# Kernel optimization log

Hardware: AMD Instinct MI355X
Metric: run time of the kernel (lower is better)

## Reference

```python
import jax, jax.numpy as jnp
import numpy as np

B, T, D = 4, 2048, 1024
H = 16
DK = D // H


def setup_inputs() -> dict:
    key = jax.random.key(0)
    k1, k2, k3, k4 = jax.random.split(key, 4)
    x = jax.random.normal(k1, (B, T, D), dtype=jnp.float32)
    prefix_lengths = jax.random.randint(k2, (B,), 0, 1024, dtype=jnp.int64)
    # torch Linear weights: [out_features, in_features], scaled like kaiming-uniform-ish
    W_qkv = jax.random.normal(k3, (3 * D, D), dtype=jnp.float32) / np.sqrt(D)
    W_o = jax.random.normal(k4, (D, D), dtype=jnp.float32) / np.sqrt(D)
    return {"x": x, "prefix_lengths": prefix_lengths, "W_qkv": W_qkv, "W_o": W_o}


def _prefix_lm_mask(seq_len, prefix_lengths):
    # True where attention is BLOCKED.
    pos = jnp.arange(seq_len)
    key_pos = pos[None, None, :]          # [1,1,T]
    query_pos = pos[None, :, None]        # [1,T,1]
    prefix = prefix_lengths[:, None, None]  # [B,1,1]
    q_in_pre = query_pos < prefix
    k_in_pre = key_pos < prefix
    block_pre_to_suf = q_in_pre & ~k_in_pre
    block_future_suf = ~q_in_pre & ~k_in_pre & (key_pos > query_pos)
    return block_pre_to_suf | block_future_suf  # [B,T,T]


def reference(x, prefix_lengths, W_qkv, W_o):
    Bb, Tt, Cc = x.shape
    qkv = x @ W_qkv.T                     # [B,T,3D]
    qkv = qkv.reshape(Bb, Tt, 3, H, DK).transpose(2, 0, 3, 1, 4)  # [3,B,H,T,dk]
    q, k, v = qkv[0], qkv[1], qkv[2]
    scale = 1.0 / np.sqrt(DK).astype(np.float32)
    attn = jnp.einsum('bhqd,bhkd->bhqk', q, k) * scale  # [B,H,T,T]
    pl = jnp.clip(prefix_lengths.astype(jnp.int32), 0, Tt)
    mask = _prefix_lm_mask(Tt, pl)        # [B,T,T]
    attn = jnp.where(mask[:, None, :, :], -jnp.inf, attn)
    attn = jax.nn.softmax(attn, axis=-1)
    out = jnp.einsum('bhqk,bhkd->bhqd', attn, v)  # [B,H,T,dk]
    out = out.transpose(0, 2, 1, 3).reshape(Bb, Tt, Cc)
    return out @ W_o.T
```

## Files before the change

kernel.cpp:

```cpp
#include <hip/hip_runtime.h>
#include <stdint.h>

#define NB 4
#define NT 2048
#define ND 1024
#define NH 16
#define NDK 64
#define NTD 3072

typedef __attribute__((ext_vector_type(8))) short short8;
typedef __attribute__((ext_vector_type(4))) float f32x4;
typedef unsigned short u16;
typedef unsigned int u32;

__device__ __forceinline__ u16 f2bf(float f) {
    u32 u = __builtin_bit_cast(u32, f);
    u += 0x7fffu + ((u >> 16) & 1u);
    return (u16)(u >> 16);
}
__device__ __forceinline__ float bf2f(u16 s) {
    u32 u = ((u32)s) << 16;
    return __builtin_bit_cast(float, u);
}

__device__ __forceinline__ void gl_lds16(const u16* g, u16* l) {
    __builtin_amdgcn_global_load_lds(
        (const __attribute__((address_space(1))) u32*)g,
        (__attribute__((address_space(3))) u32*)l, 16, 0, 0);
}

__device__ __forceinline__ int swz(int row, int col) {
    return row * 32 + ((((col >> 3) ^ (row >> 1) ^ (row >> 3)) & 3) << 3) + (col & 7);
}

__global__ __launch_bounds__(256) void cvt_all(const float* __restrict__ x,
                                               const float* __restrict__ wqkv,
                                               const float* __restrict__ wo,
                                               u16* __restrict__ xb,
                                               u16* __restrict__ wqb,
                                               u16* __restrict__ wob) {
    const int n0 = NB * NT * ND;
    const int n1 = 3 * ND * ND;
    int i = (blockIdx.x * 256 + threadIdx.x) * 8;
    const float* src;
    u16* dst;
    if (i < n0) {
        src = x + i; dst = xb + i;
    } else if (i < n0 + n1) {
        src = wqkv + (i - n0); dst = wqb + (i - n0);
    } else {
        src = wo + (i - n0 - n1); dst = wob + (i - n0 - n1);
    }
    float4 a = *(const float4*)(src);
    float4 b = *(const float4*)(src + 4);
    short8 r;
    r[0] = (short)f2bf(a.x); r[1] = (short)f2bf(a.y);
    r[2] = (short)f2bf(a.z); r[3] = (short)f2bf(a.w);
    r[4] = (short)f2bf(b.x); r[5] = (short)f2bf(b.y);
    r[6] = (short)f2bf(b.z); r[7] = (short)f2bf(b.w);
    *(short8*)(dst) = r;
}

template <typename OutT>
__global__ __launch_bounds__(256) void gemm_bt(const u16* __restrict__ A,
                                               const u16* __restrict__ Bm,
                                               OutT* __restrict__ C,
                                               int M, int N, int K) {
    __shared__ __align__(16) u16 As[128 * 32];
    __shared__ __align__(16) u16 Bs[128 * 32];
    const int tid  = threadIdx.x;
    const int wave = tid >> 6, lane = tid & 63;
    const int quad = lane >> 4, l16 = lane & 15;
    const int wm = wave >> 1, wn = wave & 1;
    const int row0 = blockIdx.x * 128, col0 = blockIdx.y * 128;

    f32x4 acc[4][4];
#pragma unroll
    for (int i = 0; i < 4; ++i)
#pragma unroll
        for (int j = 0; j < 4; ++j) acc[i][j] = (f32x4){0.f, 0.f, 0.f, 0.f};

    const u16* Ag = A + (size_t)(row0 + (tid >> 2)) * K + ((tid & 3) * 8);
    const u16* Bg = Bm + (size_t)(col0 + (tid >> 2)) * K + ((tid & 3) * 8);
    const size_t stride64 = (size_t)64 * K;
    u16* As0 = As + wave * 512;
    u16* As1 = As + 2048 + wave * 512;
    u16* Bs0 = Bs + wave * 512;
    u16* Bs1 = Bs + 2048 + wave * 512;

    for (int k0 = 0; k0 < K; k0 += 32) {
        gl_lds16(Ag + k0, As0);
        gl_lds16(Ag + k0 + stride64, As1);
        gl_lds16(Bg + k0, Bs0);
        gl_lds16(Bg + k0 + stride64, Bs1);
        __syncthreads();
        short8 af[4], bfr[4];
#pragma unroll
        for (int mi = 0; mi < 4; ++mi)
            af[mi] = *(const short8*)&As[(wm * 64 + mi * 16 + l16) * 32 + quad * 8];
#pragma unroll
        for (int ni = 0; ni < 4; ++ni)
            bfr[ni] = *(const short8*)&Bs[(wn * 64 + ni * 16 + l16) * 32 + quad * 8];
#pragma unroll
        for (int mi = 0; mi < 4; ++mi)
#pragma unroll
            for (int ni = 0; ni < 4; ++ni)
                acc[mi][ni] = __builtin_amdgcn_mfma_f32_16x16x32_bf16(
                    af[mi], bfr[ni], acc[mi][ni], 0, 0, 0);
        __syncthreads();
    }

#pragma unroll
    for (int mi = 0; mi < 4; ++mi) {
#pragma unroll
        for (int ni = 0; ni < 4; ++ni) {
            const int r = row0 + wm * 64 + mi * 16 + quad * 4;
            const int c = col0 + wn * 64 + ni * 16 + l16;
#pragma unroll
            for (int rr = 0; rr < 4; ++rr) {
                float v = acc[mi][ni][rr];
                if constexpr (sizeof(OutT) == 2)
                    C[(size_t)(r + rr) * N + c] = (OutT)f2bf(v);
                else
                    C[(size_t)(r + rr) * N + c] = (OutT)v;
            }
        }
    }
}

__global__ __launch_bounds__(256) void transpose_v(const u16* __restrict__ qkv,
                                                   u16* __restrict__ vt) {
    __shared__ __align__(16) u16 L[64 * 72];
    const int tid = threadIdx.x;
    const int bh = blockIdx.x, b = bh >> 4, h = bh & 15;
    const int t0 = blockIdx.y * 64;
    const u16* Vg = qkv + ((size_t)(b * NT + t0)) * NTD + 2 * ND + h * NDK;

    const int trow = tid >> 3, g = tid & 7;
#pragma unroll
    for (int rep = 0; rep < 2; ++rep) {
        const int t = trow + rep * 32;
        short8 v = *(const short8*)(Vg + (size_t)t * NTD + g * 8);
        *(short8*)&L[t * 72 + ((g ^ (t & 7)) << 3)] = v;
    }
    __syncthreads();
    const int d = tid & 63, w = tid >> 6;
    u16* O = vt + ((size_t)bh * 64 + d) * NT + t0;
#pragma unroll
    for (int rep = 0; rep < 2; ++rep) {
        const int c = w + rep * 4;
        short8 o;
#pragma unroll
        for (int j = 0; j < 8; ++j) {
            const int t = c * 8 + j;
            o[j] = L[t * 72 + ((((d >> 3) ^ (t & 7)) << 3)) + (d & 7)];
        }
        *(short8*)(O + c * 8) = o;
    }
}

__global__ __launch_bounds__(256) void flash_prefix(const u16* __restrict__ qkv,
                                                    const u16* __restrict__ vt,
                                                    const int* __restrict__ plen,
                                                    u16* __restrict__ attn) {
    __shared__ __align__(16) u16 Vt2[2][2048];
    __shared__ __align__(16) u16 Kt2[2][2048];
    __shared__ __align__(16) u16 Pl[4 * 512];

    const int tid  = threadIdx.x;
    const int wave = tid >> 6, lane = tid & 63;
    const int quad = lane >> 4, l16 = lane & 15;
    const int bh = blockIdx.x, b = bh >> 4, h = bh & 15;
    const int q0 = blockIdx.y * 64;

    int P;
    {
        bool is64 = (plen[1] == 0) && (plen[3] == 0);
        P = is64 ? plen[2 * b] : plen[b];
        P = P < 0 ? 0 : (P > NT ? NT : P);
    }

    const u16* Qg = qkv + (size_t)b * NT * NTD + h * NDK;
    const u16* Kg = Qg + ND;
    const u16* Vtb = vt + (size_t)bh * 64 * NT;

    const int qbase = q0 + wave * 16;
    u16* Pw = Pl + wave * 512;

    const float QSCALE = 0.18033688f;

    const int va = tid;
    const int vrow = va >> 2;
    const int vtq = (va ^ (vrow >> 1) ^ (vrow >> 3)) & 3;
    const u16* vsrc = Vtb + (size_t)vrow * NT + vtq * 8;
    const int ka = tid;
    const int krow = ka >> 3;
    const int kc = (ka ^ krow) & 7;
    const u16* ksrc = Kg + (size_t)krow * NTD + kc * 8;
    const int ldsoff = wave * 512;

    short8 qa[2];
#pragma unroll
    for (int kd = 0; kd < 2; ++kd) {
        short8 tq = *(const short8*)(Qg + (size_t)(qbase + l16) * NTD + kd * 32 + quad * 8);
#pragma unroll
        for (int j = 0; j < 8; ++j)
            tq[j] = (short)f2bf(bf2f((u16)tq[j]) * QSCALE);
        qa[kd] = tq;
    }

    short8 ones;
#pragma unroll
    for (int j = 0; j < 8; ++j) ones[j] = (short)0x3F80;

    f32x4 o[4];
#pragma unroll
    for (int nt = 0; nt < 4; ++nt) o[nt] = (f32x4){0.f, 0.f, 0.f, 0.f};
    f32x4 lsum = (f32x4){0.f, 0.f, 0.f, 0.f};

    int kl[4];
#pragma unroll
    for (int rr = 0; rr < 4; ++rr) {
        const int qrow = qbase + quad * 4 + rr;
        kl[rr] = (qrow < P) ? P : (qrow + 1);
    }
    const int klmin = (qbase < P) ? P : (qbase + 1);
    const int kmax = (q0 + 64 > P) ? (q0 + 64) : P;

    gl_lds16(vsrc, &Vt2[0][ldsoff]);
    gl_lds16(ksrc, &Kt2[0][ldsoff]);
    int buf = 0;

    for (int k0 = 0; k0 < kmax; k0 += 32) {
        __syncthreads();
        if (k0 + 32 < kmax) {
            gl_lds16(vsrc + (k0 + 32), &Vt2[buf ^ 1][ldsoff]);
            gl_lds16(ksrc + (size_t)(k0 + 32) * NTD, &Kt2[buf ^ 1][ldsoff]);
        }
        const u16* Kb = Kt2[buf];
        const u16* Vb = Vt2[buf];

        f32x4 s[2];
#pragma unroll
        for (int ni = 0; ni < 2; ++ni) {
            s[ni] = (f32x4){0.f, 0.f, 0.f, 0.f};
#pragma unroll
            for (int kd = 0; kd < 2; ++kd) {
                const int r = ni * 16 + l16;
                const short8 kb = *(const short8*)&Kb[r * 64 + ((((kd * 4 + quad) ^ r) & 7) << 3)];
                s[ni] = __builtin_amdgcn_mfma_f32_16x16x32_bf16(qa[kd], kb, s[ni], 0, 0, 0);
            }
        }

        const bool full = (k0 + 32 <= klmin);
#pragma unroll
        for (int ni = 0; ni < 2; ++ni) {
#pragma unroll
            for (int rr = 0; rr < 4; ++rr) {
                float sv = s[ni][rr];
                if (!full) {
                    const int kpos = k0 + ni * 16 + l16;
                    sv = (kpos < kl[rr]) ? sv : -1e30f;
                }
                const float p = exp2f(sv);
                const u32 u = __builtin_bit_cast(u32, p) + 0x8000u;
                Pw[swz(quad * 4 + rr, ni * 16 + l16)] = (u16)(u >> 16);
            }
        }

        const short8 pa = *(const short8*)&Pw[swz(l16, quad * 8)];
        lsum = __builtin_amdgcn_mfma_f32_16x16x32_bf16(pa, ones, lsum, 0, 0, 0);
#pragma unroll
        for (int nt = 0; nt < 4; ++nt) {
            const short8 vb = *(const short8*)&Vb[swz(nt * 16 + l16, quad * 8)];
            o[nt] = __builtin_amdgcn_mfma_f32_16x16x32_bf16(pa, vb, o[nt], 0, 0, 0);
        }
        buf ^= 1;
    }

#pragma unroll
    for (int rr = 0; rr < 4; ++rr) {
        const float inv = 1.0f / lsum[rr];
        const size_t rowoff = (size_t)(b * NT + qbase + quad * 4 + rr) * ND + h * NDK;
#pragma unroll
        for (int nt = 0; nt < 4; ++nt)
            attn[rowoff + nt * 16 + l16] = f2bf(o[nt][rr] * inv);
    }
}

extern "C" void kernel_launch(void* const* d_in, const int* in_sizes, int n_in,
                              void* d_out, int out_size, void* d_ws, size_t ws_size,
                              hipStream_t stream) {
    const float* x    = (const float*)d_in[0];
    const int*   plen = (const int*)d_in[1];
    const float* wqkv = (const float*)d_in[2];
    const float* wo   = (const float*)d_in[3];
    float* out = (float*)d_out;

    char* ws = (char*)d_ws;
    u16* xb   = (u16*)(ws);
    u16* wqb  = (u16*)(ws + 16777216);
    u16* wob  = (u16*)(ws + 23068672);
    u16* qkv  = (u16*)(ws + 25165824);
    u16* attn = (u16*)(ws + 75497472);
    u16* vtb  = (u16*)(ws + 92274688);

    cvt_all<<<6144, 256, 0, stream>>>(x, wqkv, wo, xb, wqb, wob);

    gemm_bt<u16><<<dim3(64, 24), 256, 0, stream>>>(xb, wqb, qkv, NB * NT, 3 * ND, ND);

    transpose_v<<<dim3(64, 32), 256, 0, stream>>>(qkv, vtb);

    flash_prefix<<<dim3(64, 32), 256, 0, stream>>>(qkv, vtb, plen, attn);

    gemm_bt<float><<<dim3(64, 8), 256, 0, stream>>>(attn, wob, out, NB * NT, ND, ND);
}
```

Before: 300.1 us.

## Split key range across wave pairs with 32-query tiles and LDS reduction

Each block now covers 32 query rows instead of 64. The four waves form two pairs that each process half of a 64-key tile, and their partial outputs and row sums are combined through LDS at the end. The grid doubles and is launched in reverse query order so the long causal blocks start first, which should improve load balance and occupancy. The cost is an extra LDS reduction and barrier, and K/V tiles are loaded twice as often per query row.

```diff
diff --git a/kernel.cpp b/kernel.cpp
--- a/kernel.cpp
+++ b/kernel.cpp
@@ -163,15 +163,16 @@
                                                     const u16* __restrict__ vt,
                                                     const int* __restrict__ plen,
                                                     u16* __restrict__ attn) {
-    __shared__ __align__(16) u16 Vt2[2][2048];
-    __shared__ __align__(16) u16 Kt2[2][2048];
+    __shared__ __align__(16) u16 Kt2[2][4096];
+    __shared__ __align__(16) u16 Vt2[2][4096];
     __shared__ __align__(16) u16 Pl[4 * 512];
 
     const int tid  = threadIdx.x;
     const int wave = tid >> 6, lane = tid & 63;
     const int quad = lane >> 4, l16 = lane & 15;
+    const int pair = wave >> 1, rg = wave & 1;
     const int bh = blockIdx.x, b = bh >> 4, h = bh & 15;
-    const int q0 = blockIdx.y * 64;
+    const int q0 = (63 - blockIdx.y) * 32;
 
     int P;
     {
@@ -184,20 +185,15 @@
     const u16* Kg = Qg + ND;
     const u16* Vtb = vt + (size_t)bh * 64 * NT;
 
-    const int qbase = q0 + wave * 16;
+    const int qbase = q0 + rg * 16;
     u16* Pw = Pl + wave * 512;
-
     const float QSCALE = 0.18033688f;
 
-    const int va = tid;
-    const int vrow = va >> 2;
-    const int vtq = (va ^ (vrow >> 1) ^ (vrow >> 3)) & 3;
-    const u16* vsrc = Vtb + (size_t)vrow * NT + vtq * 8;
-    const int ka = tid;
-    const int krow = ka >> 3;
-    const int kc = (ka ^ krow) & 7;
-    const u16* ksrc = Kg + (size_t)krow * NTD + kc * 8;
-    const int ldsoff = wave * 512;
+    const int krow = tid >> 3, kch = (tid ^ krow) & 7;
+    const u16* ksp = Kg + (size_t)krow * NTD + kch * 8;
+    const int vd = tid >> 3, vch = (tid ^ vd) & 7;
+    const u16* vsp = Vtb + (size_t)vd * NT + vch * 8;
+    const int koff = wave * 512;
 
     short8 qa[2];
 #pragma unroll
@@ -225,17 +221,25 @@
         kl[rr] = (qrow < P) ? P : (qrow + 1);
     }
     const int klmin = (qbase < P) ? P : (qbase + 1);
-    const int kmax = (q0 + 64 > P) ? (q0 + 64) : P;
-
-    gl_lds16(vsrc, &Vt2[0][ldsoff]);
-    gl_lds16(ksrc, &Kt2[0][ldsoff]);
+    const int kmax = (q0 + 32 > P) ? (q0 + 32) : P;
+
+    gl_lds16(ksp, &Kt2[0][koff]);
+    gl_lds16(ksp + (size_t)32 * NTD, &Kt2[0][2048 + koff]);
+    gl_lds16(vsp, &Vt2[0][koff]);
+    gl_lds16(vsp + (size_t)32 * NT, &Vt2[0][2048 + koff]);
+    const u16* ksn = ksp + (size_t)64 * NTD;
+    const u16* vsn = vsp + 64;
     int buf = 0;
 
-    for (int k0 = 0; k0 < kmax; k0 += 32) {
+    for (int k0 = 0; k0 < kmax; k0 += 64) {
         __syncthreads();
-        if (k0 + 32 < kmax) {
-            gl_lds16(vsrc + (k0 + 32), &Vt2[buf ^ 1][ldsoff]);
-            gl_lds16(ksrc + (size_t)(k0 + 32) * NTD, &Kt2[buf ^ 1][ldsoff]);
+        if (k0 + 64 < kmax) {
+            gl_lds16(ksn, &Kt2[buf ^ 1][koff]);
+            gl_lds16(ksn + (size_t)32 * NTD, &Kt2[buf ^ 1][2048 + koff]);
+            gl_lds16(vsn, &Vt2[buf ^ 1][koff]);
+            gl_lds16(vsn + (size_t)32 * NT, &Vt2[buf ^ 1][2048 + koff]);
+            ksn += (size_t)64 * NTD;
+            vsn += 64;
         }
         const u16* Kb = Kt2[buf];
         const u16* Vb = Vt2[buf];
@@ -244,22 +248,22 @@
 #pragma unroll
         for (int ni = 0; ni < 2; ++ni) {
             s[ni] = (f32x4){0.f, 0.f, 0.f, 0.f};
+            const int r = pair * 32 + ni * 16 + l16;
 #pragma unroll
             for (int kd = 0; kd < 2; ++kd) {
-                const int r = ni * 16 + l16;
-                const short8 kb = *(const short8*)&Kb[r * 64 + ((((kd * 4 + quad) ^ r) & 7) << 3)];
+                const short8 kb = *(const short8*)&Kb[r * 64 + ((((kd * 4 + quad) ^ (l16 & 7)) & 7) << 3)];
                 s[ni] = __builtin_amdgcn_mfma_f32_16x16x32_bf16(qa[kd], kb, s[ni], 0, 0, 0);
             }
         }
 
-        const bool full = (k0 + 32 <= klmin);
+        const bool full = (k0 + pair * 32 + 32 <= klmin);
 #pragma unroll
         for (int ni = 0; ni < 2; ++ni) {
 #pragma unroll
             for (int rr = 0; rr < 4; ++rr) {
                 float sv = s[ni][rr];
                 if (!full) {
-                    const int kpos = k0 + ni * 16 + l16;
+                    const int kpos = k0 + pair * 32 + ni * 16 + l16;
                     sv = (kpos < kl[rr]) ? sv : -1e30f;
                 }
                 const float p = exp2f(sv);
@@ -272,19 +276,47 @@
         lsum = __builtin_amdgcn_mfma_f32_16x16x32_bf16(pa, ones, lsum, 0, 0, 0);
 #pragma unroll
         for (int nt = 0; nt < 4; ++nt) {
-            const short8 vb = *(const short8*)&Vb[swz(nt * 16 + l16, quad * 8)];
+            const int d = nt * 16 + l16;
+            const short8 vb = *(const short8*)&Vb[d * 64 + ((((pair * 4 + quad) ^ (l16 & 7)) & 7) << 3)];
             o[nt] = __builtin_amdgcn_mfma_f32_16x16x32_bf16(pa, vb, o[nt], 0, 0, 0);
         }
         buf ^= 1;
     }
 
-#pragma unroll
-    for (int rr = 0; rr < 4; ++rr) {
-        const float inv = 1.0f / lsum[rr];
-        const size_t rowoff = (size_t)(b * NT + qbase + quad * 4 + rr) * ND + h * NDK;
+    __syncthreads();
+    float* comb = (float*)&Kt2[0][0];
+    if (wave >= 2) {
+        float* cw = comb + (wave - 2) * 1056;
 #pragma unroll
         for (int nt = 0; nt < 4; ++nt)
-            attn[rowoff + nt * 16 + l16] = f2bf(o[nt][rr] * inv);
+#pragma unroll
+            for (int rr = 0; rr < 4; ++rr)
+                cw[(quad * 4 + rr) * 65 + nt * 16 + l16] = o[nt][rr];
+        if (l16 == 0) {
+#pragma unroll
+            for (int rr = 0; rr < 4; ++rr)
+                cw[1040 + quad * 4 + rr] = lsum[rr];
+        }
+    }
+    __syncthreads();
+    if (wave < 2) {
+        const float* cw = comb + wave * 1056;
+#pragma unroll
+        for (int rr = 0; rr < 4; ++rr)
+            lsum[rr] += cw[1040 + quad * 4 + rr];
+#pragma unroll
+        for (int nt = 0; nt < 4; ++nt)
+#pragma unroll
+            for (int rr = 0; rr < 4; ++rr)
+                o[nt][rr] += cw[(quad * 4 + rr) * 65 + nt * 16 + l16];
+#pragma unroll
+        for (int rr = 0; rr < 4; ++rr) {
+            const float inv = 1.0f / lsum[rr];
+            const size_t rowoff = (size_t)(b * NT + qbase + quad * 4 + rr) * ND + h * NDK;
+#pragma unroll
+            for (int nt = 0; nt < 4; ++nt)
+                attn[rowoff + nt * 16 + l16] = f2bf(o[nt][rr] * inv);
+        }
     }
 }
 
@@ -311,7 +343,7 @@
 
     transpose_v<<<dim3(64, 32), 256, 0, stream>>>(qkv, vtb);
 
-    flash_prefix<<<dim3(64, 32), 256, 0, stream>>>(qkv, vtb, plen, attn);
+    flash_prefix<<<dim3(64, 64), 256, 0, stream>>>(qkv, vtb, plen, attn);
 
     gemm_bt<float><<<dim3(64, 8), 256, 0, stream>>>(attn, wob, out, NB * NT, ND, ND);
 }
```

Result: slower. 308.3 us (+2.7%).

## Fuse V transpose into QKV GEMM epilogue and use persistent atomic scheduling for attention

Applied to the files above, without the earlier changes.

The separate transpose_v kernel is removed. A specialized QKV GEMM writes the V columns straight into a transposed layout through an LDS staging step in its epilogue. The flash attention kernel becomes persistent with 1024 blocks, and each block takes tasks from a global atomic counter, starting with the longest query tiles, to balance the triangular causal workload. This costs an extra memset, an atomic per task, and a counter placed just before the attn buffer in the workspace.

```diff
diff --git a/kernel.cpp b/kernel.cpp
--- a/kernel.cpp
+++ b/kernel.cpp
@@ -128,163 +128,233 @@
     }
 }
 
-__global__ __launch_bounds__(256) void transpose_v(const u16* __restrict__ qkv,
-                                                   u16* __restrict__ vt) {
-    __shared__ __align__(16) u16 L[64 * 72];
-    const int tid = threadIdx.x;
-    const int bh = blockIdx.x, b = bh >> 4, h = bh & 15;
-    const int t0 = blockIdx.y * 64;
-    const u16* Vg = qkv + ((size_t)(b * NT + t0)) * NTD + 2 * ND + h * NDK;
-
-    const int trow = tid >> 3, g = tid & 7;
-#pragma unroll
-    for (int rep = 0; rep < 2; ++rep) {
-        const int t = trow + rep * 32;
-        short8 v = *(const short8*)(Vg + (size_t)t * NTD + g * 8);
-        *(short8*)&L[t * 72 + ((g ^ (t & 7)) << 3)] = v;
-    }
-    __syncthreads();
-    const int d = tid & 63, w = tid >> 6;
-    u16* O = vt + ((size_t)bh * 64 + d) * NT + t0;
-#pragma unroll
-    for (int rep = 0; rep < 2; ++rep) {
-        const int c = w + rep * 4;
-        short8 o;
-#pragma unroll
-        for (int j = 0; j < 8; ++j) {
-            const int t = c * 8 + j;
-            o[j] = L[t * 72 + ((((d >> 3) ^ (t & 7)) << 3)) + (d & 7)];
-        }
-        *(short8*)(O + c * 8) = o;
+__global__ __launch_bounds__(256) void gemm_qkv(const u16* __restrict__ A,
+                                                const u16* __restrict__ Bm,
+                                                u16* __restrict__ Cq,
+                                                u16* __restrict__ vtb) {
+    const int Kd = ND, Nn = NTD;
+    __shared__ __align__(16) u16 As[128 * 32];
+    __shared__ __align__(16) u16 Bs[128 * 32];
+    const int tid  = threadIdx.x;
+    const int wave = tid >> 6, lane = tid & 63;
+    const int quad = lane >> 4, l16 = lane & 15;
+    const int wm = wave >> 1, wn = wave & 1;
+    const int row0 = blockIdx.x * 128, col0 = blockIdx.y * 128;
+
+    f32x4 acc[4][4];
+#pragma unroll
+    for (int i = 0; i < 4; ++i)
+#pragma unroll
+        for (int j = 0; j < 4; ++j) acc[i][j] = (f32x4){0.f, 0.f, 0.f, 0.f};
+
+    const u16* Ag = A + (size_t)(row0 + (tid >> 2)) * Kd + ((tid & 3) * 8);
+    const u16* Bg = Bm + (size_t)(col0 + (tid >> 2)) * Kd + ((tid & 3) * 8);
+    const size_t stride64 = (size_t)64 * Kd;
+    u16* As0 = As + wave * 512;
+    u16* As1 = As + 2048 + wave * 512;
+    u16* Bs0 = Bs + wave * 512;
+    u16* Bs1 = Bs + 2048 + wave * 512;
+
+    for (int k0 = 0; k0 < Kd; k0 += 32) {
+        gl_lds16(Ag + k0, As0);
+        gl_lds16(Ag + k0 + stride64, As1);
+        gl_lds16(Bg + k0, Bs0);
+        gl_lds16(Bg + k0 + stride64, Bs1);
+        __syncthreads();
+        short8 af[4], bfr[4];
+#pragma unroll
+        for (int mi = 0; mi < 4; ++mi)
+            af[mi] = *(const short8*)&As[(wm * 64 + mi * 16 + l16) * 32 + quad * 8];
+#pragma unroll
+        for (int ni = 0; ni < 4; ++ni)
+            bfr[ni] = *(const short8*)&Bs[(wn * 64 + ni * 16 + l16) * 32 + quad * 8];
+#pragma unroll
+        for (int mi = 0; mi < 4; ++mi)
+#pragma unroll
+            for (int ni = 0; ni < 4; ++ni)
+                acc[mi][ni] = __builtin_amdgcn_mfma_f32_16x16x32_bf16(
+                    af[mi], bfr[ni], acc[mi][ni], 0, 0, 0);
+        __syncthreads();
+    }
+
+    if (col0 < 2048) {
+#pragma unroll
+        for (int mi = 0; mi < 4; ++mi)
+#pragma unroll
+            for (int ni = 0; ni < 4; ++ni) {
+                const int r = row0 + wm * 64 + mi * 16 + quad * 4;
+                const int c = col0 + wn * 64 + ni * 16 + l16;
+#pragma unroll
+                for (int rr = 0; rr < 4; ++rr)
+                    Cq[(size_t)(r + rr) * Nn + c] = f2bf(acc[mi][ni][rr]);
+            }
+    } else {
+        const int hb = ((col0 - 2048) >> 6) + wn;
+        const int bq = (row0 + wm * 64) >> 11;
+        const int tb = (row0 + wm * 64) & 2047;
+        u16* Ovt = vtb + (size_t)(bq * NH + hb) * 64 * NT + tb;
+#pragma unroll
+        for (int phase = 0; phase < 2; ++phase) {
+            __syncthreads();
+            if ((wave >> 1) == phase) {
+                u16* L = (wave & 1) ? Bs : As;
+#pragma unroll
+                for (int mi = 0; mi < 4; ++mi) {
+                    const int r4 = mi * 4 + quad;
+#pragma unroll
+                    for (int ni = 0; ni < 4; ++ni) {
+                        const int cl = ni * 16 + l16;
+                        u32 lo = (u32)f2bf(acc[mi][ni][0]) | ((u32)f2bf(acc[mi][ni][1]) << 16);
+                        u32 hi = (u32)f2bf(acc[mi][ni][2]) | ((u32)f2bf(acc[mi][ni][3]) << 16);
+                        u32* p = (u32*)&L[cl * 64 + (((r4 ^ cl) & 15) << 2)];
+                        p[0] = lo; p[1] = hi;
+                    }
+                }
+#pragma unroll
+                for (int rep = 0; rep < 8; ++rep) {
+                    const int cl = (lane >> 3) + rep * 8;
+                    const int tc = lane & 7;
+                    const u32* p0 = (const u32*)&L[cl * 64 + ((((2 * tc) ^ cl) & 15) << 2)];
+                    const u32* p1 = (const u32*)&L[cl * 64 + ((((2 * tc + 1) ^ cl) & 15) << 2)];
+                    u32 o0 = p0[0], o1 = p0[1], o2 = p1[0], o3 = p1[1];
+                    u32* q = (u32*)(Ovt + (size_t)cl * NT + tc * 8);
+                    q[0] = o0; q[1] = o1; q[2] = o2; q[3] = o3;
+                }
+            }
+        }
     }
 }
 
 __global__ __launch_bounds__(256) void flash_prefix(const u16* __restrict__ qkv,
                                                     const u16* __restrict__ vt,
                                                     const int* __restrict__ plen,
-                                                    u16* __restrict__ attn) {
+                                                    u16* __restrict__ attn,
+                                                    u32* __restrict__ ctr) {
     __shared__ __align__(16) u16 Vt2[2][2048];
     __shared__ __align__(16) u16 Kt2[2][2048];
     __shared__ __align__(16) u16 Pl[4 * 512];
+    __shared__ int taskS;
 
     const int tid  = threadIdx.x;
     const int wave = tid >> 6, lane = tid & 63;
     const int quad = lane >> 4, l16 = lane & 15;
-    const int bh = blockIdx.x, b = bh >> 4, h = bh & 15;
-    const int q0 = blockIdx.y * 64;
-
-    int P;
-    {
-        bool is64 = (plen[1] == 0) && (plen[3] == 0);
-        P = is64 ? plen[2 * b] : plen[b];
+    const float QSCALE = 0.18033688f;
+    const int ldsoff = wave * 512;
+
+    short8 ones;
+#pragma unroll
+    for (int j = 0; j < 8; ++j) ones[j] = (short)0x3F80;
+
+    const bool is64 = (plen[1] == 0) && (plen[3] == 0);
+
+    for (;;) {
+        if (tid == 0) taskS = (int)atomicAdd(ctr, 1u);
+        __syncthreads();
+        const int task = taskS;
+        if (task >= 2048) break;
+
+        const int bh = task & 63, b = bh >> 4, h = bh & 15;
+        const int q0 = (31 - (task >> 6)) * 64;
+
+        int P = is64 ? plen[2 * b] : plen[b];
         P = P < 0 ? 0 : (P > NT ? NT : P);
-    }
-
-    const u16* Qg = qkv + (size_t)b * NT * NTD + h * NDK;
-    const u16* Kg = Qg + ND;
-    const u16* Vtb = vt + (size_t)bh * 64 * NT;
-
-    const int qbase = q0 + wave * 16;
-    u16* Pw = Pl + wave * 512;
-
-    const float QSCALE = 0.18033688f;
-
-    const int va = tid;
-    const int vrow = va >> 2;
-    const int vtq = (va ^ (vrow >> 1) ^ (vrow >> 3)) & 3;
-    const u16* vsrc = Vtb + (size_t)vrow * NT + vtq * 8;
-    const int ka = tid;
-    const int krow = ka >> 3;
-    const int kc = (ka ^ krow) & 7;
-    const u16* ksrc = Kg + (size_t)krow * NTD + kc * 8;
-    const int ldsoff = wave * 512;
-
-    short8 qa[2];
-#pragma unroll
-    for (int kd = 0; kd < 2; ++kd) {
-        short8 tq = *(const short8*)(Qg + (size_t)(qbase + l16) * NTD + kd * 32 + quad * 8);
-#pragma unroll
-        for (int j = 0; j < 8; ++j)
-            tq[j] = (short)f2bf(bf2f((u16)tq[j]) * QSCALE);
-        qa[kd] = tq;
-    }
-
-    short8 ones;
-#pragma unroll
-    for (int j = 0; j < 8; ++j) ones[j] = (short)0x3F80;
-
-    f32x4 o[4];
-#pragma unroll
-    for (int nt = 0; nt < 4; ++nt) o[nt] = (f32x4){0.f, 0.f, 0.f, 0.f};
-    f32x4 lsum = (f32x4){0.f, 0.f, 0.f, 0.f};
-
-    int kl[4];
-#pragma unroll
-    for (int rr = 0; rr < 4; ++rr) {
-        const int qrow = qbase + quad * 4 + rr;
-        kl[rr] = (qrow < P) ? P : (qrow + 1);
-    }
-    const int klmin = (qbase < P) ? P : (qbase + 1);
-    const int kmax = (q0 + 64 > P) ? (q0 + 64) : P;
-
-    gl_lds16(vsrc, &Vt2[0][ldsoff]);
-    gl_lds16(ksrc, &Kt2[0][ldsoff]);
-    int buf = 0;
-
-    for (int k0 = 0; k0 < kmax; k0 += 32) {
-        __syncthreads();
-        if (k0 + 32 < kmax) {
-            gl_lds16(vsrc + (k0 + 32), &Vt2[buf ^ 1][ldsoff]);
-            gl_lds16(ksrc + (size_t)(k0 + 32) * NTD, &Kt2[buf ^ 1][ldsoff]);
-        }
-        const u16* Kb = Kt2[buf];
-        const u16* Vb = Vt2[buf];
-
-        f32x4 s[2];
-#pragma unroll
-        for (int ni = 0; ni < 2; ++ni) {
-            s[ni] = (f32x4){0.f, 0.f, 0.f, 0.f};
-#pragma unroll
-            for (int kd = 0; kd < 2; ++kd) {
-                const int r = ni * 16 + l16;
-                const short8 kb = *(const short8*)&Kb[r * 64 + ((((kd * 4 + quad) ^ r) & 7) << 3)];
-                s[ni] = __builtin_amdgcn_mfma_f32_16x16x32_bf16(qa[kd], kb, s[ni], 0, 0, 0);
-            }
-        }
-
-        const bool full = (k0 + 32 <= klmin);
-#pragma unroll
-        for (int ni = 0; ni < 2; ++ni) {
-#pragma unroll
-            for (int rr = 0; rr < 4; ++rr) {
-                float sv = s[ni][rr];
-                if (!full) {
-                    const int kpos = k0 + ni * 16 + l16;
-                    sv = (kpos < kl[rr]) ? sv : -1e30f;
+
+        const u16* Qg = qkv + (size_t)b * NT * NTD + h * NDK;
+        const u16* Kg = Qg + ND;
+        const u16* Vtb = vt + (size_t)bh * 64 * NT;
+        const int qbase = q0 + wave * 16;
+        u16* Pw = Pl + wave * 512;
+
+        const int vrow = tid >> 2;
+        const int vtq = (tid ^ (vrow >> 1) ^ (vrow >> 3)) & 3;
+        const u16* vsrc = Vtb + (size_t)vrow * NT + vtq * 8;
+        const int krow = tid >> 3;
+        const int kc = (tid ^ krow) & 7;
+        const u16* ksrc = Kg + (size_t)krow * NTD + kc * 8;
+
+        short8 qa[2];
+#pragma unroll
+        for (int kd = 0; kd < 2; ++kd) {
+            short8 tq = *(const short8*)(Qg + (size_t)(qbase + l16) * NTD + kd * 32 + quad * 8);
+#pragma unroll
+            for (int j = 0; j < 8; ++j)
+                tq[j] = (short)f2bf(bf2f((u16)tq[j]) * QSCALE);
+            qa[kd] = tq;
+        }
+
+        f32x4 o[4];
+#pragma unroll
+        for (int nt = 0; nt < 4; ++nt) o[nt] = (f32x4){0.f, 0.f, 0.f, 0.f};
+        f32x4 lsum = (f32x4){0.f, 0.f, 0.f, 0.f};
+
+        int kl[4];
+#pragma unroll
+        for (int rr = 0; rr < 4; ++rr) {
+            const int qrow = qbase + quad * 4 + rr;
+            kl[rr] = (qrow < P) ? P : (qrow + 1);
+        }
+        const int klmin = (qbase < P) ? P : (qbase + 1);
+        const int kmax = (q0 + 64 > P) ? (q0 + 64) : P;
+
+        gl_lds16(vsrc, &Vt2[0][ldsoff]);
+        gl_lds16(ksrc, &Kt2[0][ldsoff]);
+        int buf = 0;
+
+        for (int k0 = 0; k0 < kmax; k0 += 32) {
+            __syncthreads();
+            if (k0 + 32 < kmax) {
+                gl_lds16(vsrc + (k0 + 32), &Vt2[buf ^ 1][ldsoff]);
+                gl_lds16(ksrc + (size_t)(k0 + 32) * NTD, &Kt2[buf ^ 1][ldsoff]);
+            }
+            const u16* Kb = Kt2[buf];
+            const u16* Vb = Vt2[buf];
+
+            f32x4 s[2];
+#pragma unroll
+            for (int ni = 0; ni < 2; ++ni) {
+                s[ni] = (f32x4){0.f, 0.f, 0.f, 0.f};
+#pragma unroll
+                for (int kd = 0; kd < 2; ++kd) {
+                    const int r = ni * 16 + l16;
+                    const short8 kb = *(const short8*)&Kb[r * 64 + ((((kd * 4 + quad) ^ r) & 7) << 3)];
+                    s[ni] = __builtin_amdgcn_mfma_f32_16x16x32_bf16(qa[kd], kb, s[ni], 0, 0, 0);
                 }
-                const float p = exp2f(sv);
-                const u32 u = __builtin_bit_cast(u32, p) + 0x8000u;
-                Pw[swz(quad * 4 + rr, ni * 16 + l16)] = (u16)(u >> 16);
-            }
-        }
-
-        const short8 pa = *(const short8*)&Pw[swz(l16, quad * 8)];
-        lsum = __builtin_amdgcn_mfma_f32_16x16x32_bf16(pa, ones, lsum, 0, 0, 0);
-#pragma unroll
-        for (int nt = 0; nt < 4; ++nt) {
-            const short8 vb = *(const short8*)&Vb[swz(nt * 16 + l16, quad * 8)];
-            o[nt] = __builtin_amdgcn_mfma_f32_16x16x32_bf16(pa, vb, o[nt], 0, 0, 0);
-        }
-        buf ^= 1;
-    }
-
-#pragma unroll
-    for (int rr = 0; rr < 4; ++rr) {
-        const float inv = 1.0f / lsum[rr];
-        const size_t rowoff = (size_t)(b * NT + qbase + quad * 4 + rr) * ND + h * NDK;
-#pragma unroll
-        for (int nt = 0; nt < 4; ++nt)
-            attn[rowoff + nt * 16 + l16] = f2bf(o[nt][rr] * inv);
+            }
+
+            const bool full = (k0 + 32 <= klmin);
+#pragma unroll
+            for (int ni = 0; ni < 2; ++ni) {
+#pragma unroll
+                for (int rr = 0; rr < 4; ++rr) {
+                    float sv = s[ni][rr];
+                    if (!full) {
+                        const int kpos = k0 + ni * 16 + l16;
+                        sv = (kpos < kl[rr]) ? sv : -1e30f;
+                    }
+                    const float p = exp2f(sv);
+                    const u32 u = __builtin_bit_cast(u32, p) + 0x8000u;
+                    Pw[swz(quad * 4 + rr, ni * 16 + l16)] = (u16)(u >> 16);
+                }
+            }
+
+            const short8 pa = *(const short8*)&Pw[swz(l16, quad * 8)];
+            lsum = __builtin_amdgcn_mfma_f32_16x16x32_bf16(pa, ones, lsum, 0, 0, 0);
+#pragma unroll
+            for (int nt = 0; nt < 4; ++nt) {
+                const short8 vb = *(const short8*)&Vb[swz(nt * 16 + l16, quad * 8)];
+                o[nt] = __builtin_amdgcn_mfma_f32_16x16x32_bf16(pa, vb, o[nt], 0, 0, 0);
+            }
+            buf ^= 1;
+        }
+
+#pragma unroll
+        for (int rr = 0; rr < 4; ++rr) {
+            const float inv = 1.0f / lsum[rr];
+            const size_t rowoff = (size_t)(b * NT + qbase + quad * 4 + rr) * ND + h * NDK;
+#pragma unroll
+            for (int nt = 0; nt < 4; ++nt)
+                attn[rowoff + nt * 16 + l16] = f2bf(o[nt][rr] * inv);
+        }
     }
 }
 
@@ -304,14 +374,15 @@
     u16* qkv  = (u16*)(ws + 25165824);
     u16* attn = (u16*)(ws + 75497472);
     u16* vtb  = (u16*)(ws + 92274688);
+    u32* ctr  = (u32*)(ws + 75497468);
+
+    hipMemsetAsync(ctr, 0, 4, stream);
 
     cvt_all<<<6144, 256, 0, stream>>>(x, wqkv, wo, xb, wqb, wob);
 
-    gemm_bt<u16><<<dim3(64, 24), 256, 0, stream>>>(xb, wqb, qkv, NB * NT, 3 * ND, ND);
-
-    transpose_v<<<dim3(64, 32), 256, 0, stream>>>(qkv, vtb);
-
-    flash_prefix<<<dim3(64, 32), 256, 0, stream>>>(qkv, vtb, plen, attn);
+    gemm_qkv<<<dim3(64, 24), 256, 0, stream>>>(xb, wqb, qkv, vtb);
+
+    flash_prefix<<<1024, 256, 0, stream>>>(qkv, vtb, plen, attn, ctr);
 
     gemm_bt<float><<<dim3(64, 8), 256, 0, stream>>>(attn, wob, out, NB * NT, ND, ND);
 }
```

Result: no change. 305.5 us (+1.8%).
